# Optimization experiments

Measured on AMD Instinct MI355X. Metric: run time of the kernel, lower is better.

The kernel has to match this reference:

```python
import jax, jax.numpy as jnp
import numpy as np

TAU = 2.0
V_TH = 1.0


def setup_inputs() -> dict:
    key = jax.random.key(0)
    k1, k2, k3 = jax.random.split(key, 3)
    T, B, N = 128, 64, 1024
    x = jax.random.normal(k1, (T, B, N), dtype=jnp.float32)
    # nn.Linear(hidden, hidden, bias=False) weights: [out, in]
    scale = 1.0 / np.sqrt(N)
    W1 = jax.random.uniform(k2, (N, N), dtype=jnp.float32, minval=-scale, maxval=scale)
    W2 = jax.random.uniform(k3, (N, N), dtype=jnp.float32, minval=-scale, maxval=scale)
    return {"x": x, "W1": W1, "W2": W2}


def _lif_scan(h_seq):
    # h_seq: [T, B, N]; LIF recurrence with tau=2, v_th=1, reset v = h*(1-s)
    def step(v, x_t):
        h = v + (x_t - v) / TAU
        s = (h >= V_TH).astype(h.dtype)
        return h * (1.0 - s), s

    v0 = jnp.zeros(h_seq.shape[1:], dtype=h_seq.dtype)
    _, spikes = jax.lax.scan(step, v0, h_seq)
    return spikes  # [T, B, N]


def reference(x, W1, W2):
    # fc1: y = x @ W1^T (torch Linear convention)
    h = jnp.einsum('tbn,mn->tbm', x, W1)
    spike = _lif_scan(h)
    return jnp.einsum('tbn,mn->tbm', spike, W2)
```

## Files before the change

### kernel.cpp

```cpp
#include <hip/hip_runtime.h>
#include <hip/hip_bf16.h>
#include <stdint.h>


#define TT 128
#define BB 64
#define NN 1024
#define MROWS (TT * BB)
#define SROW  (BB * NN)
#define MiB   ((size_t)1048576)

typedef _Float16 h8  __attribute__((ext_vector_type(8)));
typedef _Float16 h4v __attribute__((ext_vector_type(4)));
typedef float    f4  __attribute__((ext_vector_type(4)));
typedef float    v2f __attribute__((ext_vector_type(2)));

#if __has_builtin(__builtin_elementwise_fma)
#define V2FMA(a, b, c) __builtin_elementwise_fma((a), (b), (c))
#else
static __device__ __forceinline__ v2f v2fma_(v2f a, v2f b, v2f c) {
    v2f r; r[0] = fmaf(a[0], b[0], c[0]); r[1] = fmaf(a[1], b[1], c[1]); return r;
}
#define V2FMA(a, b, c) v2fma_((a), (b), (c))
#endif

#define GL2LDS(g, l) __builtin_amdgcn_global_load_lds(                         \
    (const __attribute__((address_space(1))) void*)(const void*)(g),           \
    (__attribute__((address_space(3))) void*)(void*)(l), 16, 0, 0)

__global__ __launch_bounds__(256) void prep(const float* __restrict__ W1,
                                            const float* __restrict__ W2,
                                            _Float16* __restrict__ B0, _Float16* __restrict__ B1,
                                            float* __restrict__ W2T) {
    const int nb = blockIdx.x;
    const int tid = threadIdx.x;
    if (nb < 1024) {
        const int i = nb * 256 + tid;
        const float4 v = reinterpret_cast<const float4*>(W1)[i];
        const float f[4] = {v.x, v.y, v.z, v.w};
        h4v a0, a1;
#pragma unroll
        for (int j = 0; j < 4; ++j) {
            const _Float16 c = (_Float16)f[j];
            a0[j] = c;
            a1[j] = (_Float16)((f[j] - (float)c) * 4096.0f);
        }
        reinterpret_cast<h4v*>(B0)[i] = a0;
        reinterpret_cast<h4v*>(B1)[i] = a1;
    } else {
        __shared__ float tile[32][33];
        const int tIdx = nb - 1024;
        const int bx = (tIdx & 31) * 32, by = (tIdx >> 5) * 32;
        const int tx = tid & 31, ty = tid >> 5;
#pragma unroll
        for (int j = 0; j < 32; j += 8)
            tile[ty + j][tx] = W2[(size_t)(by + ty + j) * NN + bx + tx];
        __syncthreads();
#pragma unroll
        for (int j = 0; j < 32; j += 8)
            W2T[(size_t)(bx + ty + j) * NN + by + tx] = tile[tx][ty + j];
    }
}

__global__ __launch_bounds__(256, 2) void gemm_split(const float* __restrict__ X,
                                                     const _Float16* __restrict__ B0g,
                                                     const _Float16* __restrict__ B1g,
                                                     float* __restrict__ C) {
    __shared__ float    As[2][4096];
    __shared__ _Float16 Bs0[2][4096], Bs1[2][4096];
    const int tid  = threadIdx.x;
    const int lane = tid & 63;
    const int wid  = tid >> 6;
    const int wr   = wid >> 1, wc = wid & 1;

    const int ib = blockIdx.x;
    const int p  = ((ib >> 6) << 3) + (ib & 7);
    const int cc = (ib >> 3) & 7;
    const int rowBase = p * 128;
    const int colBase = cc * 128;

    const size_t aOff = (size_t)(rowBase + wid * 32 + (lane >> 3)) * NN
                      + (((lane & 7) ^ (lane >> 3)) << 2);
    const int ldsA = wid * 1024;

    const int srowB = wid * 32 + (lane >> 2);
    const size_t bOff = (size_t)(colBase + srowB) * NN
                      + (((lane & 3) ^ ((srowB >> 1) & 3)) << 3);
    const int ldsB = wid * 1024;

    int fA0[4], fA1[4], fB[4];
#pragma unroll
    for (int i = 0; i < 4; ++i) {
        const int ra = wr * 64 + i * 16 + (lane & 15);
        const int rb = wc * 64 + i * 16 + (lane & 15);
        const int ca = (lane >> 4) * 2;
        fA0[i] = ra * 32 + (((ca + 0) ^ (ra & 7)) << 2);
        fA1[i] = ra * 32 + (((ca + 1) ^ (ra & 7)) << 2);
        fB[i]  = rb * 32 + (((lane >> 4) ^ ((rb >> 1) & 3)) << 3);
    }

    f4 acc0[4][4], acc1[4][4];
#pragma unroll
    for (int i = 0; i < 4; ++i)
#pragma unroll
        for (int j = 0; j < 4; ++j) { acc0[i][j] = (f4)0.0f; acc1[i][j] = (f4)0.0f; }

#define STAGE(bi, K0)                                              \
    do {                                                           \
        GL2LDS(X + aOff + (size_t)0  * NN + (K0), &As[bi][ldsA]);          \
        GL2LDS(X + aOff + (size_t)8  * NN + (K0), &As[bi][ldsA + 256]);    \
        GL2LDS(X + aOff + (size_t)16 * NN + (K0), &As[bi][ldsA + 512]);    \
        GL2LDS(X + aOff + (size_t)24 * NN + (K0), &As[bi][ldsA + 768]);    \
        GL2LDS(B0g + bOff + (K0),                  &Bs0[bi][ldsB]);        \
        GL2LDS(B0g + bOff + (size_t)16 * NN + (K0), &Bs0[bi][ldsB + 512]); \
        GL2LDS(B1g + bOff + (K0),                  &Bs1[bi][ldsB]);        \
        GL2LDS(B1g + bOff + (size_t)16 * NN + (K0), &Bs1[bi][ldsB + 512]); \
    } while (0)

    STAGE(0, 0);
    __syncthreads();

    const int NT = NN / 32;
    for (int t = 0; t < NT; ++t) {
        const int cur = t & 1;
        if (t < NT - 1) STAGE(cur ^ 1, (t + 1) * 32);

        h8 a0f[4], a1f[4], b0f[4], b1f[4];
#pragma unroll
        for (int i = 0; i < 4; ++i) {
            const f4 lo = *(const f4*)&As[cur][fA0[i]];
            const f4 hi = *(const f4*)&As[cur][fA1[i]];
#pragma unroll
            for (int e = 0; e < 4; ++e) {
                const float fl = lo[e], fh = hi[e];
                const _Float16 cl = (_Float16)fl, ch = (_Float16)fh;
                a0f[i][e]     = cl;
                a0f[i][4 + e] = ch;
                a1f[i][e]     = (_Float16)((fl - (float)cl) * 4096.0f);
                a1f[i][4 + e] = (_Float16)((fh - (float)ch) * 4096.0f);
            }
            b0f[i] = *(const h8*)&Bs0[cur][fB[i]];
            b1f[i] = *(const h8*)&Bs1[cur][fB[i]];
        }
#pragma unroll
        for (int i = 0; i < 4; ++i)
#pragma unroll
            for (int j = 0; j < 4; ++j) {
                acc0[i][j] = __builtin_amdgcn_mfma_f32_16x16x32_f16(a0f[i], b0f[j], acc0[i][j], 0, 0, 0);
                acc1[i][j] = __builtin_amdgcn_mfma_f32_16x16x32_f16(a0f[i], b1f[j], acc1[i][j], 0, 0, 0);
                acc1[i][j] = __builtin_amdgcn_mfma_f32_16x16x32_f16(a1f[i], b0f[j], acc1[i][j], 0, 0, 0);
            }
        __syncthreads();
    }
#undef STAGE

    const int orow = rowBase + wr * 64 + (lane >> 4) * 4;
    const int ocol = colBase + wc * 64 + (lane & 15);
#pragma unroll
    for (int i = 0; i < 4; ++i)
#pragma unroll
        for (int j = 0; j < 4; ++j)
#pragma unroll
            for (int q = 0; q < 4; ++q)
                C[(size_t)(orow + i * 16 + q) * NN + ocol + j * 16] =
                    acc0[i][j][q] + acc1[i][j][q] * (1.0f / 4096.0f);
}

__global__ __launch_bounds__(256) void lif_scan(const float* __restrict__ H,
                                                unsigned long long* __restrict__ mask) {
    const int g = blockIdx.x * 256 + threadIdx.x;
    const int b = g >> 10;
    const int n = g & 1023;
    const int word = n >> 6;
    const bool lane0 = (threadIdx.x & 63) == 0;

    float v = 0.0f;
    float buf[16];
#pragma unroll
    for (int j = 0; j < 16; ++j) buf[j] = H[(size_t)j * SROW + g];

    for (int t0 = 0; t0 < TT; t0 += 16) {
        float nbuf[16];
        if (t0 + 16 < TT) {
#pragma unroll
            for (int j = 0; j < 16; ++j) nbuf[j] = H[(size_t)(t0 + 16 + j) * SROW + g];
        } else {
#pragma unroll
            for (int j = 0; j < 16; ++j) nbuf[j] = 0.f;
        }
#pragma unroll
        for (int j = 0; j < 16; ++j) {
            const float x = buf[j];
            const float h = v + (x - v) * 0.5f;
            const bool s = (h >= 1.0f);
            v = s ? 0.0f : h;
            const unsigned long long m = __ballot(s);
            if (lane0) mask[((size_t)(t0 + j) * BB + b) * 16 + word] = m;
        }
#pragma unroll
        for (int j = 0; j < 16; ++j) buf[j] = nbuf[j];
    }
}

__global__ __launch_bounds__(256) void spike_matmul(const unsigned long long* __restrict__ mask,
                                                    const float* __restrict__ W2T,
                                                    float* __restrict__ out) {
    __shared__ unsigned long long sw[16];
    const int r = blockIdx.x;
    const int tid = threadIdx.x;
    if (tid < 16) sw[tid] = mask[(size_t)r * 16 + tid];
    __syncthreads();

    f4 acc = (f4)0.0f;
#pragma unroll 1
    for (int w = 0; w < 16; ++w) {
        unsigned long long bits = sw[w];
        while (bits) {
            const int n = w * 64 + (__ffsll(bits) - 1);
            bits &= bits - 1;
            const f4 rv = reinterpret_cast<const f4*>(W2T + (size_t)n * NN)[tid];
            acc[0] += rv[0]; acc[1] += rv[1]; acc[2] += rv[2]; acc[3] += rv[3];
        }
    }
    reinterpret_cast<f4*>(out + (size_t)r * NN)[tid] = acc;
}

__global__ __launch_bounds__(256) void transpose_nn(const float* __restrict__ in,
                                                    float* __restrict__ out) {
    __shared__ float tile[32][33];
    const int bx = blockIdx.x * 32, by = blockIdx.y * 32;
    const int tx = threadIdx.x, ty = threadIdx.y;
#pragma unroll
    for (int j = 0; j < 32; j += 8)
        tile[ty + j][tx] = in[(size_t)(by + ty + j) * NN + bx + tx];
    __syncthreads();
#pragma unroll
    for (int j = 0; j < 32; j += 8)
        out[(size_t)(bx + ty + j) * NN + by + tx] = tile[tx][ty + j];
}

#define BM 128
#define BN 64
#define BK 16
__global__ __launch_bounds__(256, 4) void gemm1_f32(const float* __restrict__ A,
                                                    const float* __restrict__ B,
                                                    float* __restrict__ C) {
    __shared__ float Asb[2][BK][132];
    __shared__ float Bsb[2][BK][68];
    const int tid = threadIdx.x;
    const int ty = tid >> 4;
    const int tx = tid & 15;
    const int rowBase = blockIdx.y * BM;
    const int colBase = blockIdx.x * BN;
    const int sr = tid >> 2;
    const int sk = (tid & 3) * 4;

    const float* Ap0 = A + (size_t)(rowBase + sr) * NN + sk;
    const float* Ap1 = Ap0 + (size_t)64 * NN;
    const float* Bp  = B + (size_t)(colBase + sr) * NN + sk;

    v2f acc[4][4];
#pragma unroll
    for (int i = 0; i < 4; ++i)
#pragma unroll
        for (int j = 0; j < 4; ++j) acc[i][j] = (v2f){0.f, 0.f};

    float4 ra0 = *(const float4*)Ap0;
    float4 ra1 = *(const float4*)Ap1;
    float4 rb  = *(const float4*)Bp;

#define STW(buf)                                                                       \
    do {                                                                               \
        Asb[buf][sk + 0][sr] = ra0.x; Asb[buf][sk + 1][sr] = ra0.y;                    \
        Asb[buf][sk + 2][sr] = ra0.z; Asb[buf][sk + 3][sr] = ra0.w;                    \
        Asb[buf][sk + 0][sr + 64] = ra1.x; Asb[buf][sk + 1][sr + 64] = ra1.y;          \
        Asb[buf][sk + 2][sr + 64] = ra1.z; Asb[buf][sk + 3][sr + 64] = ra1.w;          \
        Bsb[buf][sk + 0][sr] = rb.x;  Bsb[buf][sk + 1][sr] = rb.y;                     \
        Bsb[buf][sk + 2][sr] = rb.z;  Bsb[buf][sk + 3][sr] = rb.w;                     \
    } while (0)

    STW(0);
    __syncthreads();
    const int NT = NN / BK;
    for (int t = 0; t < NT; ++t) {
        const int cur = t & 1;
        if (t < NT - 1) {
            const int ko = (t + 1) * BK;
            ra0 = *(const float4*)(Ap0 + ko);
            ra1 = *(const float4*)(Ap1 + ko);
            rb  = *(const float4*)(Bp + ko);
        }
#pragma unroll
        for (int k = 0; k < BK; ++k) {
            const v2f* ap = (const v2f*)&Asb[cur][k][ty * 8];
            const float4 bf = *(const float4*)&Bsb[cur][k][tx * 4];
            const float bb[4] = {bf.x, bf.y, bf.z, bf.w};
            const v2f a0 = ap[0], a1 = ap[1], a2 = ap[2], a3 = ap[3];
#pragma unroll
            for (int j = 0; j < 4; ++j) {
                const v2f bd = {bb[j], bb[j]};
                acc[0][j] = V2FMA(a0, bd, acc[0][j]);
                acc[1][j] = V2FMA(a1, bd, acc[1][j]);
                acc[2][j] = V2FMA(a2, bd, acc[2][j]);
                acc[3][j] = V2FMA(a3, bd, acc[3][j]);
            }
        }
        if (t < NT - 1) STW(cur ^ 1);
        __syncthreads();
    }
#undef STW
    float* Cp = C + (size_t)(rowBase + ty * 8) * NN + colBase + tx * 4;
#pragma unroll
    for (int rp = 0; rp < 4; ++rp) {
        float4 lo = {acc[rp][0][0], acc[rp][1][0], acc[rp][2][0], acc[rp][3][0]};
        float4 hi = {acc[rp][0][1], acc[rp][1][1], acc[rp][2][1], acc[rp][3][1]};
        *(float4*)(Cp + (size_t)(2 * rp) * NN)     = lo;
        *(float4*)(Cp + (size_t)(2 * rp + 1) * NN) = hi;
    }
}

extern "C" void kernel_launch(void* const* d_in, const int* in_sizes, int n_in,
                              void* d_out, int out_size, void* d_ws, size_t ws_size,
                              hipStream_t stream) {
    const float* x  = (const float*)d_in[0];
    const float* W1 = (const float*)d_in[1];
    const float* W2 = (const float*)d_in[2];
    float* out = (float*)d_out;

    unsigned long long* mask = (unsigned long long*)d_ws;
    float* W2T = (float*)((char*)d_ws + 1 * MiB);

    if (ws_size >= 9 * MiB) {
        _Float16* B0 = (_Float16*)((char*)d_ws + 5 * MiB);
        _Float16* B1 = (_Float16*)((char*)d_ws + 7 * MiB);

        prep<<<2048, 256, 0, stream>>>(W1, W2, B0, B1, W2T);
        gemm_split<<<512, 256, 0, stream>>>(x, B0, B1, out);
    } else {
        transpose_nn<<<dim3(32, 32), dim3(32, 8), 0, stream>>>(W2, W2T);
        gemm1_f32<<<dim3(NN / BN, MROWS / BM), 256, 0, stream>>>(x, W1, out);
    }
    lif_scan<<<SROW / 256, 256, 0, stream>>>(out, mask);
    spike_matmul<<<MROWS, 256, 0, stream>>>(mask, W2T, out);
}
```

Before: 179.4 us.

## Convert X tile to split fp16 once per stage via register staging

```diff
diff --git a/kernel.cpp b/kernel.cpp
--- a/kernel.cpp
+++ b/kernel.cpp
@@ -62,41 +62,38 @@
     }
 }
 
-__global__ __launch_bounds__(256, 2) void gemm_split(const float* __restrict__ X,
-                                                     const _Float16* __restrict__ B0g,
-                                                     const _Float16* __restrict__ B1g,
-                                                     float* __restrict__ C) {
-    __shared__ float    As[2][4096];
+__global__ __launch_bounds__(256, 2) void gemm_rs(const float* __restrict__ X,
+                                                  const _Float16* __restrict__ B0g,
+                                                  const _Float16* __restrict__ B1g,
+                                                  float* __restrict__ C) {
+    __shared__ _Float16 As0[2][4096], As1[2][4096];
     __shared__ _Float16 Bs0[2][4096], Bs1[2][4096];
-    const int tid  = threadIdx.x;
-    const int lane = tid & 63;
-    const int wid  = tid >> 6;
-    const int wr   = wid >> 1, wc = wid & 1;
-
+    const int tid = threadIdx.x, lane = tid & 63, wid = tid >> 6;
+    const int wr = wid >> 1, wc = wid & 1;
     const int ib = blockIdx.x;
     const int p  = ((ib >> 6) << 3) + (ib & 7);
     const int cc = (ib >> 3) & 7;
-    const int rowBase = p * 128;
-    const int colBase = cc * 128;
-
-    const size_t aOff = (size_t)(rowBase + wid * 32 + (lane >> 3)) * NN
-                      + (((lane & 7) ^ (lane >> 3)) << 2);
-    const int ldsA = wid * 1024;
-
-    const int srowB = wid * 32 + (lane >> 2);
-    const size_t bOff = (size_t)(colBase + srowB) * NN
-                      + (((lane & 3) ^ ((srowB >> 1) & 3)) << 3);
-    const int ldsB = wid * 1024;
-
-    int fA0[4], fA1[4], fB[4];
+    const int rowBase = p * 128, colBase = cc * 128;
+
+    const int sr = wid * 32 + (lane >> 2);
+    const int sc = lane & 3;
+    const size_t xOff = (size_t)(rowBase + sr) * NN + sc * 8;
+    const int wsw = (sc ^ ((sr >> 1) & 3)) << 3;
+    const int wA0 = sr * 32 + wsw;
+    const int wA1 = (sr + 16) * 32 + wsw;
+
+    const int swzB = (((lane & 3) ^ ((sr >> 1) & 3)) << 3);
+    const size_t bOff0 = (size_t)(colBase + sr) * NN + swzB;
+    const size_t bOff1 = bOff0 + (size_t)16 * NN;
+    const int l0 = wid * 1024, l1 = l0 + 512;
+
+    int fA[4], fB[4];
 #pragma unroll
     for (int i = 0; i < 4; ++i) {
         const int ra = wr * 64 + i * 16 + (lane & 15);
         const int rb = wc * 64 + i * 16 + (lane & 15);
-        const int ca = (lane >> 4) * 2;
-        fA0[i] = ra * 32 + (((ca + 0) ^ (ra & 7)) << 2);
-        fA1[i] = ra * 32 + (((ca + 1) ^ (ra & 7)) << 2);
-        fB[i]  = rb * 32 + (((lane >> 4) ^ ((rb >> 1) & 3)) << 3);
+        fA[i] = ra * 32 + (((lane >> 4) ^ ((ra >> 1) & 3)) << 3);
+        fB[i] = rb * 32 + (((lane >> 4) ^ ((rb >> 1) & 3)) << 3);
     }
 
     f4 acc0[4][4], acc1[4][4];
@@ -105,40 +102,62 @@
 #pragma unroll
         for (int j = 0; j < 4; ++j) { acc0[i][j] = (f4)0.0f; acc1[i][j] = (f4)0.0f; }
 
-#define STAGE(bi, K0)                                              \
-    do {                                                           \
-        GL2LDS(X + aOff + (size_t)0  * NN + (K0), &As[bi][ldsA]);          \
-        GL2LDS(X + aOff + (size_t)8  * NN + (K0), &As[bi][ldsA + 256]);    \
-        GL2LDS(X + aOff + (size_t)16 * NN + (K0), &As[bi][ldsA + 512]);    \
-        GL2LDS(X + aOff + (size_t)24 * NN + (K0), &As[bi][ldsA + 768]);    \
-        GL2LDS(B0g + bOff + (K0),                  &Bs0[bi][ldsB]);        \
-        GL2LDS(B0g + bOff + (size_t)16 * NN + (K0), &Bs0[bi][ldsB + 512]); \
-        GL2LDS(B1g + bOff + (K0),                  &Bs1[bi][ldsB]);        \
-        GL2LDS(B1g + bOff + (size_t)16 * NN + (K0), &Bs1[bi][ldsB + 512]); \
+    f4 xa0, xa1, xb0, xb1;
+
+#define XLOAD(K0)                                              \
+    do {                                                       \
+        const size_t xo = xOff + (K0);                         \
+        xa0 = *(const f4*)(X + xo);                            \
+        xa1 = *(const f4*)(X + xo + 4);                        \
+        xb0 = *(const f4*)(X + xo + (size_t)16 * NN);          \
+        xb1 = *(const f4*)(X + xo + (size_t)16 * NN + 4);      \
     } while (0)
 
-    STAGE(0, 0);
+#define BSTAGE(bi, K0)                                         \
+    do {                                                       \
+        GL2LDS(B0g + bOff0 + (K0), &Bs0[bi][l0]);              \
+        GL2LDS(B0g + bOff1 + (K0), &Bs0[bi][l1]);              \
+        GL2LDS(B1g + bOff0 + (K0), &Bs1[bi][l0]);              \
+        GL2LDS(B1g + bOff1 + (K0), &Bs1[bi][l1]);              \
+    } while (0)
+
+#define AWRITE(bi)                                                             \
+    do {                                                                       \
+        h8 hi, lo;                                                             \
+        _Pragma("unroll") for (int e = 0; e < 4; ++e) {                        \
+            const float f0 = xa0[e], f1 = xa1[e];                              \
+            const _Float16 c0 = (_Float16)f0, c1 = (_Float16)f1;               \
+            hi[e] = c0; hi[4 + e] = c1;                                        \
+            lo[e]     = (_Float16)((f0 - (float)c0) * 4096.0f);                \
+            lo[4 + e] = (_Float16)((f1 - (float)c1) * 4096.0f);                \
+        }                                                                      \
+        *(h8*)&As0[bi][wA0] = hi; *(h8*)&As1[bi][wA0] = lo;                    \
+        _Pragma("unroll") for (int e = 0; e < 4; ++e) {                        \
+            const float f0 = xb0[e], f1 = xb1[e];                              \
+            const _Float16 c0 = (_Float16)f0, c1 = (_Float16)f1;               \
+            hi[e] = c0; hi[4 + e] = c1;                                        \
+            lo[e]     = (_Float16)((f0 - (float)c0) * 4096.0f);                \
+            lo[4 + e] = (_Float16)((f1 - (float)c1) * 4096.0f);                \
+        }                                                                      \
+        *(h8*)&As0[bi][wA1] = hi; *(h8*)&As1[bi][wA1] = lo;                    \
+    } while (0)
+
+    XLOAD(0);
+    BSTAGE(0, 0);
+    AWRITE(0);
     __syncthreads();
 
-    const int NT = NN / 32;
-    for (int t = 0; t < NT; ++t) {
+    for (int t = 0; t < 32; ++t) {
         const int cur = t & 1;
-        if (t < NT - 1) STAGE(cur ^ 1, (t + 1) * 32);
-
+        if (t < 31) {
+            XLOAD((t + 1) * 32);
+            BSTAGE(cur ^ 1, (t + 1) * 32);
+        }
         h8 a0f[4], a1f[4], b0f[4], b1f[4];
 #pragma unroll
         for (int i = 0; i < 4; ++i) {
-            const f4 lo = *(const f4*)&As[cur][fA0[i]];
-            const f4 hi = *(const f4*)&As[cur][fA1[i]];
-#pragma unroll
-            for (int e = 0; e < 4; ++e) {
-                const float fl = lo[e], fh = hi[e];
-                const _Float16 cl = (_Float16)fl, ch = (_Float16)fh;
-                a0f[i][e]     = cl;
-                a0f[i][4 + e] = ch;
-                a1f[i][e]     = (_Float16)((fl - (float)cl) * 4096.0f);
-                a1f[i][4 + e] = (_Float16)((fh - (float)ch) * 4096.0f);
-            }
+            a0f[i] = *(const h8*)&As0[cur][fA[i]];
+            a1f[i] = *(const h8*)&As1[cur][fA[i]];
             b0f[i] = *(const h8*)&Bs0[cur][fB[i]];
             b1f[i] = *(const h8*)&Bs1[cur][fB[i]];
         }
@@ -150,9 +169,12 @@
                 acc1[i][j] = __builtin_amdgcn_mfma_f32_16x16x32_f16(a0f[i], b1f[j], acc1[i][j], 0, 0, 0);
                 acc1[i][j] = __builtin_amdgcn_mfma_f32_16x16x32_f16(a1f[i], b0f[j], acc1[i][j], 0, 0, 0);
             }
+        if (t < 31) AWRITE(cur ^ 1);
         __syncthreads();
     }
-#undef STAGE
+#undef XLOAD
+#undef BSTAGE
+#undef AWRITE
 
     const int orow = rowBase + wr * 64 + (lane >> 4) * 4;
     const int ocol = colBase + wc * 64 + (lane & 15);
@@ -335,7 +357,7 @@
         _Float16* B1 = (_Float16*)((char*)d_ws + 7 * MiB);
 
         prep<<<2048, 256, 0, stream>>>(W1, W2, B0, B1, W2T);
-        gemm_split<<<512, 256, 0, stream>>>(x, B0, B1, out);
+        gemm_rs<<<512, 256, 0, stream>>>(x, B0, B1, out);
     } else {
         transpose_nn<<<dim3(32, 32), dim3(32, 8), 0, stream>>>(W2, W2T);
         gemm1_f32<<<dim3(NN / BN, MROWS / BM), 256, 0, stream>>>(x, W1, out);
```

Result: faster. 164.2 us (-8.5%).
